# Performance work log

Hardware: AMD Instinct MI355X
Metric: run time of the kernel (lower is better)

The kernel has to match this reference:

```python
import jax, jax.numpy as jnp
import numpy as np

B, N, D, R, K = 16384, 20, 64, 3, 64  # batch, triples per sample, embed dim, n_relations, r_dim


def setup_inputs() -> dict:
    key = jax.random.key(0)
    ks = jax.random.split(key, 8)
    # xavier_normal std for [2D, K] matrices: sqrt(2/(2D+K))
    std_w = float(np.sqrt(2.0 / (2 * D + K)))
    std_r = float(np.sqrt(2.0 / (R + K)))
    return {
        "u_emb": jax.random.normal(ks[0], (B, D), dtype=jnp.float32),
        "i_emb": jax.random.normal(ks[1], (B, D), dtype=jnp.float32),
        "a_emb": jax.random.normal(ks[2], (B, N, D), dtype=jnp.float32),
        "o_emb": jax.random.normal(ks[3], (B, N, D), dtype=jnp.float32),
        "s": jax.random.randint(ks[4], (B, N), 0, R, dtype=jnp.int64),
        "w_uir": jax.random.normal(ks[5], (R, 2 * D, K), dtype=jnp.float32) * std_w,
        "w_aor": jax.random.normal(ks[6], (R, 2 * D, K), dtype=jnp.float32) * std_w,
        "r_vec": jax.random.normal(ks[7], (R, K), dtype=jnp.float32) * std_r,
    }


def reference(u_emb, i_emb, a_emb, o_emb, s, w_uir, w_aor, r_vec):
    # transr predictor, bpr loss
    ui_in = jnp.concatenate([u_emb, i_emb], axis=-1)          # [B, 2D]
    ao_in = jnp.concatenate([a_emb, o_emb], axis=-1)          # [B, N, 2D]
    n_rel = w_uir.shape[0]
    ui_emb = jnp.zeros(ao_in.shape[:2] + (w_uir.shape[-1],), dtype=ui_in.dtype)  # [B, N, K]
    ao_emb = jnp.zeros_like(ui_emb)
    for r_idx in range(n_rel):  # small fixed relation count
        m = (s == r_idx)[..., None]                            # [B, N, 1]
        ui_r = ui_in @ w_uir[r_idx] + r_vec[r_idx]             # [B, K]
        ao_r = jnp.einsum("bnd,dk->bnk", ao_in, w_aor[r_idx])  # [B, N, K]
        ui_emb = jnp.where(m, ui_r[:, None, :], ui_emb)
        ao_emb = jnp.where(m, ao_r, ao_emb)
    pred = jnp.sum(ui_emb * ao_emb, axis=-1)                   # [B, N]
    return pred
```

## Files before the change

### kernel.cpp

```cpp
#include <hip/hip_runtime.h>
#include <hip/hip_bf16.h>

#define BB   16384
#define NN   20
#define NREL 3

typedef __attribute__((ext_vector_type(8))) short  short8;
typedef __attribute__((ext_vector_type(4))) float  f32x4;

__device__ __forceinline__ float lo16(unsigned int u) {
    union { unsigned int x; float f; } c; c.x = u << 16; return c.f;
}
__device__ __forceinline__ float hi16(unsigned int u) {
    union { unsigned int x; float f; } c; c.x = u & 0xFFFF0000u; return c.f;
}

__device__ __forceinline__ unsigned short f2bu(float f) {
    union { float f; unsigned int u; } x;
    x.f = f;
    unsigned int r = x.u + 0x7FFFu + ((x.u >> 16) & 1u);
    return (unsigned short)(r >> 16);
}

__global__ __launch_bounds__(256) void k_precompute(
    const float* __restrict__ w_uir,
    const float* __restrict__ w_aor,
    const float* __restrict__ r_vec,
    unsigned short* __restrict__ McatT,
    float* __restrict__ cvec)
{
    int idx = blockIdx.x * 256 + threadIdx.x;
    if (idx < NREL * 128 * 128) {
        int d = idx & 127;
        int e = (idx >> 7) & 127;
        int r = idx >> 14;
        const float4* pu = reinterpret_cast<const float4*>(w_uir + (r * 128 + d) * 64);
        const float4* pa = reinterpret_cast<const float4*>(w_aor + (r * 128 + e) * 64);
        float acc = 0.f;
        #pragma unroll
        for (int k = 0; k < 16; ++k) {
            float4 a = pu[k], b = pa[k];
            acc += a.x * b.x + a.y * b.y + a.z * b.z + a.w * b.w;
        }
        McatT[(r * 128 + e) * 128 + d] = f2bu(acc);
    } else if (idx < NREL * 128 * 128 + NREL * 128) {
        int j = idx - NREL * 128 * 128;
        int r = j >> 7, e = j & 127;
        const float4* pr = reinterpret_cast<const float4*>(r_vec + r * 64);
        const float4* pa = reinterpret_cast<const float4*>(w_aor + (r * 128 + e) * 64);
        float acc = 0.f;
        #pragma unroll
        for (int k = 0; k < 16; ++k) {
            float4 a = pr[k], b = pa[k];
            acc += a.x * b.x + a.y * b.y + a.z * b.z + a.w * b.w;
        }
        cvec[j] = acc;
    }
}

__global__ __launch_bounds__(256) void k_gemm(
    const float* __restrict__ u_emb,
    const float* __restrict__ i_emb,
    const unsigned short* __restrict__ McatT,
    const float* __restrict__ cvec,
    unsigned short* __restrict__ vp)
{
    __shared__ unsigned short Atile[64][136];
    const int t = threadIdx.x;
    const int bm = blockIdx.x & 255;
    const int bn = blockIdx.x >> 8;
    const int Mbase = bm * 64;
    const int Nbase = bn * 64;

    #pragma unroll
    for (int it = 0; it < 8; ++it) {
        int idx  = it * 256 + t;
        int row  = idx >> 5;
        int colg = idx & 31;
        const float* src = (colg < 16)
            ? (u_emb + (Mbase + row) * 64 + colg * 4)
            : (i_emb + (Mbase + row) * 64 + (colg - 16) * 4);
        float4 v = *reinterpret_cast<const float4*>(src);
        ushort4 h;
        h.x = f2bu(v.x); h.y = f2bu(v.y); h.z = f2bu(v.z); h.w = f2bu(v.w);
        *reinterpret_cast<ushort4*>(&Atile[row][colg * 4]) = h;
    }
    __syncthreads();

    const int w    = t >> 6;
    const int lane = t & 63;
    const int lr   = lane & 15;
    const int lk   = (lane >> 4) * 8;

    short8 afrag[4];
    #pragma unroll
    for (int kk = 0; kk < 4; ++kk)
        afrag[kk] = *reinterpret_cast<const short8*>(&Atile[w * 16 + lr][kk * 32 + lk]);

    #pragma unroll
    for (int nt = 0; nt < 4; ++nt) {
        f32x4 acc = {0.f, 0.f, 0.f, 0.f};
        int col = Nbase + nt * 16 + lr;
        #pragma unroll
        for (int kk = 0; kk < 4; ++kk) {
            short8 bfrag = *reinterpret_cast<const short8*>(McatT + col * 128 + kk * 32 + lk);
            acc = __builtin_amdgcn_mfma_f32_16x16x32_bf16(afrag[kk], bfrag, acc, 0, 0, 0);
        }
        float cb = cvec[col];
        #pragma unroll
        for (int reg = 0; reg < 4; ++reg) {
            int grow = Mbase + w * 16 + (lane >> 4) * 4 + reg;
            vp[grow * 384 + col] = f2bu(acc[reg] + cb);
        }
    }
}

#define K3_BLOCKS 512
#define K3_ITERS  16
#define K3_TPS    40

#define SL_A   0
#define SL_O   10240
#define SL_VP  20480
#define SL_S   22016
#define SL_SZ  22272

__device__ __forceinline__ void k3_stage(
    const float* __restrict__ a_emb, const float* __restrict__ o_emb,
    const int* __restrict__ s, const unsigned short* __restrict__ vp,
    char* L, int sidx, int wv, int lane)
{
    const size_t t0s = (size_t)sidx * K3_TPS;

    int sval = 0;
    if (wv == 2 && lane < K3_TPS) sval = s[t0s + lane];

    const char* asrc = (const char*)(a_emb + t0s * 64);
    const char* osrc = (const char*)(o_emb + t0s * 64);
    const char* vsrc = (const char*)(vp + (size_t)sidx * (2 * 3 * 128));

    if (wv < 2) {
        #pragma unroll
        for (int i = 0; i < 5; ++i) {
            int seg = i * 2 + wv;
            __builtin_amdgcn_global_load_lds(
                (const unsigned int*)(asrc + seg * 1024 + (size_t)lane * 16),
                (unsigned int*)(L + SL_A + seg * 1024), 16, 0, 0);
        }
    } else {
        #pragma unroll
        for (int i = 0; i < 5; ++i) {
            int seg = i * 2 + (wv & 1);
            __builtin_amdgcn_global_load_lds(
                (const unsigned int*)(osrc + seg * 1024 + (size_t)lane * 16),
                (unsigned int*)(L + SL_O + seg * 1024), 16, 0, 0);
        }
    }
    if (wv == 3) {
        __builtin_amdgcn_global_load_lds(
            (const unsigned int*)(vsrc + (size_t)lane * 16),
            (unsigned int*)(L + SL_VP), 16, 0, 0);
        if (lane < 32)
            __builtin_amdgcn_global_load_lds(
                (const unsigned int*)(vsrc + 1024 + (size_t)lane * 16),
                (unsigned int*)(L + SL_VP + 1024), 16, 0, 0);
    }
    if (wv == 2 && lane < K3_TPS)
        *(int*)(L + SL_S + lane * 4) = sval;
}

__device__ __forceinline__ void k3_consume(
    const char* L, int sidx, int g, int sub, float* __restrict__ out)
{
    const size_t t0s = (size_t)sidx * K3_TPS;
    #pragma unroll
    for (int p = 0; p < 3; ++p) {
        const int ltrip = p * 16 + g;
        if (p < 2 || g < 8) {
            const int bl  = ltrip / NN;
            const int sv  = *(const int*)(L + SL_S + ltrip * 4);
            const int row = bl * 3 + sv;
            float4 af = *(const float4*)(L + SL_A + ltrip * 256 + sub * 16);
            float4 of = *(const float4*)(L + SL_O + ltrip * 256 + sub * 16);
            uint2  wa = *(const uint2*)(L + SL_VP + row * 256 + sub * 8);
            uint2  wo = *(const uint2*)(L + SL_VP + row * 256 + 128 + sub * 8);
            float r = af.x * lo16(wa.x) + af.y * hi16(wa.x)
                    + af.z * lo16(wa.y) + af.w * hi16(wa.y)
                    + of.x * lo16(wo.x) + of.y * hi16(wo.x)
                    + of.z * lo16(wo.y) + of.w * hi16(wo.y);
            r += __shfl_xor(r, 1, 64);
            r += __shfl_xor(r, 2, 64);
            r += __shfl_xor(r, 4, 64);
            r += __shfl_xor(r, 8, 64);
            if (sub == 0) out[t0s + ltrip] = r;
        }
    }
}

__global__ __launch_bounds__(256) void k_pred(
    const float* __restrict__ a_emb,
    const float* __restrict__ o_emb,
    const int* __restrict__ s,
    const unsigned short* __restrict__ vp,
    float* __restrict__ out)
{
    __shared__ __align__(16) char lds[2 * SL_SZ];

    const int tid  = threadIdx.x;
    const int wv   = tid >> 6;
    const int lane = tid & 63;
    const int bid  = blockIdx.x;
    const int g    = tid >> 4;
    const int sub  = tid & 15;

    const int sbase = bid * K3_ITERS;

    k3_stage(a_emb, o_emb, s, vp, lds, sbase, wv, lane);
    __syncthreads();

    for (int it = 0; it < K3_ITERS; ++it) {
        if (it + 1 < K3_ITERS)
            k3_stage(a_emb, o_emb, s, vp, lds + ((it + 1) & 1) * SL_SZ,
                     sbase + it + 1, wv, lane);
        k3_consume(lds + (it & 1) * SL_SZ, sbase + it, g, sub, out);
        __syncthreads();
    }
}

extern "C" void kernel_launch(void* const* d_in, const int* in_sizes, int n_in,
                              void* d_out, int out_size, void* d_ws, size_t ws_size,
                              hipStream_t stream) {
    const float* u_emb = (const float*)d_in[0];
    const float* i_emb = (const float*)d_in[1];
    const float* a_emb = (const float*)d_in[2];
    const float* o_emb = (const float*)d_in[3];
    const int*   s     = (const int*)d_in[4];
    const float* w_uir = (const float*)d_in[5];
    const float* w_aor = (const float*)d_in[6];
    const float* r_vec = (const float*)d_in[7];
    float* out = (float*)d_out;

    char* ws = (char*)d_ws;
    unsigned short* McatT = (unsigned short*)ws;
    float*          cvec  = (float*)(ws + 98304);
    unsigned short* vp    = (unsigned short*)(ws + 102400);

    k_precompute<<<194, 256, 0, stream>>>(w_uir, w_aor, r_vec, McatT, cvec);
    k_gemm<<<1536, 256, 0, stream>>>(u_emb, i_emb, McatT, cvec, vp);
    k_pred<<<K3_BLOCKS, 256, 0, stream>>>(a_emb, o_emb, s, vp, out);
}
```

Baseline: 54.43 us.

## Triple-buffer k_pred with per-batch stages, explicit vmcnt waits, coalesced output

Restructures the prediction kernel to process one batch row (20 triples) per iteration across 1024 blocks, with a three-deep LDS ring filled by direct global-to-LDS loads. Fixed-count s_waitcnt vmcnt waits plus a raw s_barrier replace the full __syncthreads each iteration. Relation indices are loaded once up front, and results are staged in LDS and written out as coalesced float4 stores at the end. The aim is to keep more memory traffic in flight and cut per-iteration synchronisation. The risk is that each wave waits only on its own loads before reading buffers filled by other waves, with no barrier in between, so a read could race a load that has not landed.

```diff
diff --git a/kernel.cpp b/kernel.cpp
--- a/kernel.cpp
+++ b/kernel.cpp
@@ -115,85 +115,87 @@
     }
 }
 
-#define K3_BLOCKS 512
-#define K3_ITERS  16
-#define K3_TPS    40
-
-#define SL_A   0
-#define SL_O   10240
-#define SL_VP  20480
-#define SL_S   22016
-#define SL_SZ  22272
+#define K3_BLOCKS 1024
+#define K3_NITER  16
+#define K3_BUF    11264
+#define K3_SOFF   (3 * K3_BUF)
+#define K3_OOFF   (K3_SOFF + 1280)
+#define K3_LDS    (K3_OOFF + 1280)
 
 __device__ __forceinline__ void k3_stage(
     const float* __restrict__ a_emb, const float* __restrict__ o_emb,
-    const int* __restrict__ s, const unsigned short* __restrict__ vp,
-    char* L, int sidx, int wv, int lane)
-{
-    const size_t t0s = (size_t)sidx * K3_TPS;
-
-    int sval = 0;
-    if (wv == 2 && lane < K3_TPS) sval = s[t0s + lane];
-
-    const char* asrc = (const char*)(a_emb + t0s * 64);
-    const char* osrc = (const char*)(o_emb + t0s * 64);
-    const char* vsrc = (const char*)(vp + (size_t)sidx * (2 * 3 * 128));
-
-    if (wv < 2) {
-        #pragma unroll
-        for (int i = 0; i < 5; ++i) {
-            int seg = i * 2 + wv;
-            __builtin_amdgcn_global_load_lds(
-                (const unsigned int*)(asrc + seg * 1024 + (size_t)lane * 16),
-                (unsigned int*)(L + SL_A + seg * 1024), 16, 0, 0);
-        }
+    const unsigned short* __restrict__ vpg,
+    char* buf, int bb, int wv, int lane)
+{
+    const char* asrc = (const char*)a_emb + (size_t)bb * 5120;
+    const char* osrc = (const char*)o_emb + (size_t)bb * 5120;
+    if (wv == 0) {
+        __builtin_amdgcn_global_load_lds((const unsigned int*)(asrc + 0 * 1024 + lane * 16),
+                                         (unsigned int*)(buf + 0 * 1024), 16, 0, 0);
+        __builtin_amdgcn_global_load_lds((const unsigned int*)(asrc + 1 * 1024 + lane * 16),
+                                         (unsigned int*)(buf + 1 * 1024), 16, 0, 0);
+        __builtin_amdgcn_global_load_lds((const unsigned int*)(asrc + 2 * 1024 + lane * 16),
+                                         (unsigned int*)(buf + 2 * 1024), 16, 0, 0);
+    } else if (wv == 1) {
+        __builtin_amdgcn_global_load_lds((const unsigned int*)(asrc + 3 * 1024 + lane * 16),
+                                         (unsigned int*)(buf + 3 * 1024), 16, 0, 0);
+        __builtin_amdgcn_global_load_lds((const unsigned int*)(asrc + 4 * 1024 + lane * 16),
+                                         (unsigned int*)(buf + 4 * 1024), 16, 0, 0);
+        __builtin_amdgcn_global_load_lds((const unsigned int*)(osrc + 0 * 1024 + lane * 16),
+                                         (unsigned int*)(buf + 5120 + 0 * 1024), 16, 0, 0);
+    } else if (wv == 2) {
+        __builtin_amdgcn_global_load_lds((const unsigned int*)(osrc + 1 * 1024 + lane * 16),
+                                         (unsigned int*)(buf + 5120 + 1 * 1024), 16, 0, 0);
+        __builtin_amdgcn_global_load_lds((const unsigned int*)(osrc + 2 * 1024 + lane * 16),
+                                         (unsigned int*)(buf + 5120 + 2 * 1024), 16, 0, 0);
+        __builtin_amdgcn_global_load_lds((const unsigned int*)(osrc + 3 * 1024 + lane * 16),
+                                         (unsigned int*)(buf + 5120 + 3 * 1024), 16, 0, 0);
     } else {
-        #pragma unroll
-        for (int i = 0; i < 5; ++i) {
-            int seg = i * 2 + (wv & 1);
-            __builtin_amdgcn_global_load_lds(
-                (const unsigned int*)(osrc + seg * 1024 + (size_t)lane * 16),
-                (unsigned int*)(L + SL_O + seg * 1024), 16, 0, 0);
-        }
-    }
-    if (wv == 3) {
-        __builtin_amdgcn_global_load_lds(
-            (const unsigned int*)(vsrc + (size_t)lane * 16),
-            (unsigned int*)(L + SL_VP), 16, 0, 0);
-        if (lane < 32)
-            __builtin_amdgcn_global_load_lds(
-                (const unsigned int*)(vsrc + 1024 + (size_t)lane * 16),
-                (unsigned int*)(L + SL_VP + 1024), 16, 0, 0);
-    }
-    if (wv == 2 && lane < K3_TPS)
-        *(int*)(L + SL_S + lane * 4) = sval;
+        __builtin_amdgcn_global_load_lds((const unsigned int*)(osrc + 4 * 1024 + lane * 16),
+                                         (unsigned int*)(buf + 5120 + 4 * 1024), 16, 0, 0);
+        const char* vsrc = (const char*)vpg + (size_t)bb * 768;
+        if (lane < 48)
+            __builtin_amdgcn_global_load_lds((const unsigned int*)(vsrc + lane * 16),
+                                             (unsigned int*)(buf + 10240), 16, 0, 0);
+    }
 }
 
 __device__ __forceinline__ void k3_consume(
-    const char* L, int sidx, int g, int sub, float* __restrict__ out)
-{
-    const size_t t0s = (size_t)sidx * K3_TPS;
-    #pragma unroll
-    for (int p = 0; p < 3; ++p) {
-        const int ltrip = p * 16 + g;
-        if (p < 2 || g < 8) {
-            const int bl  = ltrip / NN;
-            const int sv  = *(const int*)(L + SL_S + ltrip * 4);
-            const int row = bl * 3 + sv;
-            float4 af = *(const float4*)(L + SL_A + ltrip * 256 + sub * 16);
-            float4 of = *(const float4*)(L + SL_O + ltrip * 256 + sub * 16);
-            uint2  wa = *(const uint2*)(L + SL_VP + row * 256 + sub * 8);
-            uint2  wo = *(const uint2*)(L + SL_VP + row * 256 + 128 + sub * 8);
-            float r = af.x * lo16(wa.x) + af.y * hi16(wa.x)
-                    + af.z * lo16(wa.y) + af.w * hi16(wa.y)
-                    + of.x * lo16(wo.x) + of.y * hi16(wo.x)
-                    + of.z * lo16(wo.y) + of.w * hi16(wo.y);
-            r += __shfl_xor(r, 1, 64);
-            r += __shfl_xor(r, 2, 64);
-            r += __shfl_xor(r, 4, 64);
-            r += __shfl_xor(r, 8, 64);
-            if (sub == 0) out[t0s + ltrip] = r;
-        }
+    char* lds, const char* buf, int it, int g, int sub)
+{
+    {
+        const int ltrip = g;
+        const int sv = *(const int*)(lds + K3_SOFF + (it * 20 + ltrip) * 4);
+        float4 af = *(const float4*)(buf + ltrip * 256 + sub * 16);
+        float4 of = *(const float4*)(buf + 5120 + ltrip * 256 + sub * 16);
+        uint2  wa = *(const uint2*)(buf + 10240 + sv * 256 + sub * 8);
+        uint2  wo = *(const uint2*)(buf + 10240 + sv * 256 + 128 + sub * 8);
+        float r = af.x * lo16(wa.x) + af.y * hi16(wa.x)
+                + af.z * lo16(wa.y) + af.w * hi16(wa.y)
+                + of.x * lo16(wo.x) + of.y * hi16(wo.x)
+                + of.z * lo16(wo.y) + of.w * hi16(wo.y);
+        r += __shfl_xor(r, 1, 64);
+        r += __shfl_xor(r, 2, 64);
+        r += __shfl_xor(r, 4, 64);
+        r += __shfl_xor(r, 8, 64);
+        if (sub == 0) *(float*)(lds + K3_OOFF + (it * 20 + ltrip) * 4) = r;
+    }
+    if (g < 4) {
+        const int ltrip = 16 + g;
+        const int sv = *(const int*)(lds + K3_SOFF + (it * 20 + ltrip) * 4);
+        float4 af = *(const float4*)(buf + ltrip * 256 + sub * 16);
+        float4 of = *(const float4*)(buf + 5120 + ltrip * 256 + sub * 16);
+        uint2  wa = *(const uint2*)(buf + 10240 + sv * 256 + sub * 8);
+        uint2  wo = *(const uint2*)(buf + 10240 + sv * 256 + 128 + sub * 8);
+        float r = af.x * lo16(wa.x) + af.y * hi16(wa.x)
+                + af.z * lo16(wa.y) + af.w * hi16(wa.y)
+                + of.x * lo16(wo.x) + of.y * hi16(wo.x)
+                + of.z * lo16(wo.y) + of.w * hi16(wo.y);
+        r += __shfl_xor(r, 1, 64);
+        r += __shfl_xor(r, 2, 64);
+        r += __shfl_xor(r, 4, 64);
+        r += __shfl_xor(r, 8, 64);
+        if (sub == 0) *(float*)(lds + K3_OOFF + (it * 20 + ltrip) * 4) = r;
     }
 }
 
@@ -201,29 +203,60 @@
     const float* __restrict__ a_emb,
     const float* __restrict__ o_emb,
     const int* __restrict__ s,
-    const unsigned short* __restrict__ vp,
+    const unsigned short* __restrict__ vpg,
     float* __restrict__ out)
 {
-    __shared__ __align__(16) char lds[2 * SL_SZ];
+    __shared__ __align__(16) char lds[K3_LDS];
 
     const int tid  = threadIdx.x;
+    const int bid  = blockIdx.x;
     const int wv   = tid >> 6;
     const int lane = tid & 63;
-    const int bid  = blockIdx.x;
     const int g    = tid >> 4;
     const int sub  = tid & 15;
-
-    const int sbase = bid * K3_ITERS;
-
-    k3_stage(a_emb, o_emb, s, vp, lds, sbase, wv, lane);
+    const size_t t0 = (size_t)bid * (K3_NITER * NN);
+    const int  b0  = bid * K3_NITER;
+
+    int sv1 = s[t0 + tid];
+    int sv2 = (tid < 64) ? s[t0 + 256 + tid] : 0;
+
+    k3_stage(a_emb, o_emb, vpg, lds + 0 * K3_BUF, b0 + 0, wv, lane);
+    k3_stage(a_emb, o_emb, vpg, lds + 1 * K3_BUF, b0 + 1, wv, lane);
+
+    *(int*)(lds + K3_SOFF + tid * 4) = sv1;
+    if (tid < 64) *(int*)(lds + K3_SOFF + 1024 + tid * 4) = sv2;
     __syncthreads();
 
-    for (int it = 0; it < K3_ITERS; ++it) {
-        if (it + 1 < K3_ITERS)
-            k3_stage(a_emb, o_emb, s, vp, lds + ((it + 1) & 1) * SL_SZ,
-                     sbase + it + 1, wv, lane);
-        k3_consume(lds + (it & 1) * SL_SZ, sbase + it, g, sub, out);
-        __syncthreads();
+    #pragma unroll
+    for (int it = 0; it < K3_NITER; ++it) {
+        if (it + 2 < K3_NITER)
+            k3_stage(a_emb, o_emb, vpg, lds + ((it + 2) % 3) * K3_BUF,
+                     b0 + it + 2, wv, lane);
+        __builtin_amdgcn_sched_barrier(0);
+
+        if (it >= 2) {
+            if (it < K3_NITER - 2) {
+                if (wv == 3) asm volatile("s_waitcnt vmcnt(4)" ::: "memory");
+                else         asm volatile("s_waitcnt vmcnt(6)" ::: "memory");
+            } else if (it == K3_NITER - 2) {
+                if (wv == 3) asm volatile("s_waitcnt vmcnt(2)" ::: "memory");
+                else         asm volatile("s_waitcnt vmcnt(3)" ::: "memory");
+            } else {
+                asm volatile("s_waitcnt vmcnt(0)" ::: "memory");
+            }
+        }
+        __builtin_amdgcn_sched_barrier(0);
+
+        k3_consume(lds, lds + (it % 3) * K3_BUF, it, g, sub);
+
+        __builtin_amdgcn_sched_barrier(0);
+        __builtin_amdgcn_s_barrier();
+    }
+
+    __syncthreads();
+    if (tid < 80) {
+        float4 v = *(const float4*)(lds + K3_OOFF + tid * 16);
+        *(float4*)(out + t0 + tid * 4) = v;
     }
 }
 
```

New measurement: 54.70 us. No clear change (+0.5%).

## Fuse projection GEMM into prediction kernel, keeping per-sample vectors in LDS

Applied to the files above, without the earlier changes.

Merges the MFMA GEMM that builds the per-sample projected vectors with the prediction kernel, so each block of 16 samples computes its vp rows into LDS and consumes them directly. This removes the global write and reread of vp and one kernel launch. The price is a loss of cross-iteration double buffering: each block now stages a/o slices in a synchronous load-then-consume pattern with extra barriers. It also launches 1024 blocks using about 56KB of LDS each.

```diff
diff --git a/kernel.cpp b/kernel.cpp
--- a/kernel.cpp
+++ b/kernel.cpp
@@ -58,172 +58,138 @@
     }
 }
 
-__global__ __launch_bounds__(256) void k_gemm(
+#define K3_BLOCKS (BB / 16)
+#define UI_OFF 0
+#define VP_OFF 4096
+#define AO_OFF 16384
+#define K3_LDS 57344
+
+__device__ __forceinline__ void stage_ao(
+    const float* __restrict__ a_emb, const float* __restrict__ o_emb,
+    char* lds, size_t t0s, int wv, int lane)
+{
+    const char* asrc = (const char*)a_emb + t0s * 256;
+    const char* osrc = (const char*)o_emb + t0s * 256;
+    #pragma unroll
+    for (int i = 0; i < 5; ++i) {
+        int seg = i * 4 + wv;
+        __builtin_amdgcn_global_load_lds(
+            (const unsigned int*)(asrc + seg * 1024 + (size_t)lane * 16),
+            (unsigned int*)(lds + AO_OFF + seg * 1024), 16, 0, 0);
+    }
+    #pragma unroll
+    for (int i = 0; i < 5; ++i) {
+        int seg = i * 4 + wv;
+        __builtin_amdgcn_global_load_lds(
+            (const unsigned int*)(osrc + seg * 1024 + (size_t)lane * 16),
+            (unsigned int*)(lds + AO_OFF + 20480 + seg * 1024), 16, 0, 0);
+    }
+}
+
+__device__ __forceinline__ void consume_slice(
+    const char* lds, int sl, size_t t0s,
+    const int* sv, int g, int sub, float* __restrict__ out)
+{
+    #pragma unroll
+    for (int p = 0; p < 5; ++p) {
+        const int ltrip = p * 16 + g;
+        const int bl    = ltrip / NN;
+        const int brow  = sl * 4 + bl;
+        const int svv   = sv[p];
+        float4 af = *(const float4*)(lds + AO_OFF + ltrip * 256 + sub * 16);
+        float4 of = *(const float4*)(lds + AO_OFF + 20480 + ltrip * 256 + sub * 16);
+        uint2  wa = *(const uint2*)(lds + VP_OFF + brow * 768 + svv * 256 + sub * 8);
+        uint2  wo = *(const uint2*)(lds + VP_OFF + brow * 768 + svv * 256 + 128 + sub * 8);
+        float r = af.x * lo16(wa.x) + af.y * hi16(wa.x)
+                + af.z * lo16(wa.y) + af.w * hi16(wa.y)
+                + of.x * lo16(wo.x) + of.y * hi16(wo.x)
+                + of.z * lo16(wo.y) + of.w * hi16(wo.y);
+        r += __shfl_xor(r, 1, 64);
+        r += __shfl_xor(r, 2, 64);
+        r += __shfl_xor(r, 4, 64);
+        r += __shfl_xor(r, 8, 64);
+        if (sub == 0) out[t0s + ltrip] = r;
+    }
+}
+
+__global__ __launch_bounds__(256) void k_fused(
     const float* __restrict__ u_emb,
     const float* __restrict__ i_emb,
-    const unsigned short* __restrict__ McatT,
-    const float* __restrict__ cvec,
-    unsigned short* __restrict__ vp)
-{
-    __shared__ unsigned short Atile[64][136];
-    const int t = threadIdx.x;
-    const int bm = blockIdx.x & 255;
-    const int bn = blockIdx.x >> 8;
-    const int Mbase = bm * 64;
-    const int Nbase = bn * 64;
-
-    #pragma unroll
-    for (int it = 0; it < 8; ++it) {
-        int idx  = it * 256 + t;
-        int row  = idx >> 5;
-        int colg = idx & 31;
-        const float* src = (colg < 16)
-            ? (u_emb + (Mbase + row) * 64 + colg * 4)
-            : (i_emb + (Mbase + row) * 64 + (colg - 16) * 4);
-        float4 v = *reinterpret_cast<const float4*>(src);
-        ushort4 h;
-        h.x = f2bu(v.x); h.y = f2bu(v.y); h.z = f2bu(v.z); h.w = f2bu(v.w);
-        *reinterpret_cast<ushort4*>(&Atile[row][colg * 4]) = h;
-    }
-    __syncthreads();
-
-    const int w    = t >> 6;
-    const int lane = t & 63;
-    const int lr   = lane & 15;
-    const int lk   = (lane >> 4) * 8;
-
-    short8 afrag[4];
-    #pragma unroll
-    for (int kk = 0; kk < 4; ++kk)
-        afrag[kk] = *reinterpret_cast<const short8*>(&Atile[w * 16 + lr][kk * 32 + lk]);
-
-    #pragma unroll
-    for (int nt = 0; nt < 4; ++nt) {
-        f32x4 acc = {0.f, 0.f, 0.f, 0.f};
-        int col = Nbase + nt * 16 + lr;
-        #pragma unroll
-        for (int kk = 0; kk < 4; ++kk) {
-            short8 bfrag = *reinterpret_cast<const short8*>(McatT + col * 128 + kk * 32 + lk);
-            acc = __builtin_amdgcn_mfma_f32_16x16x32_bf16(afrag[kk], bfrag, acc, 0, 0, 0);
-        }
-        float cb = cvec[col];
-        #pragma unroll
-        for (int reg = 0; reg < 4; ++reg) {
-            int grow = Mbase + w * 16 + (lane >> 4) * 4 + reg;
-            vp[grow * 384 + col] = f2bu(acc[reg] + cb);
-        }
-    }
-}
-
-#define K3_BLOCKS 512
-#define K3_ITERS  16
-#define K3_TPS    40
-
-#define SL_A   0
-#define SL_O   10240
-#define SL_VP  20480
-#define SL_S   22016
-#define SL_SZ  22272
-
-__device__ __forceinline__ void k3_stage(
-    const float* __restrict__ a_emb, const float* __restrict__ o_emb,
-    const int* __restrict__ s, const unsigned short* __restrict__ vp,
-    char* L, int sidx, int wv, int lane)
-{
-    const size_t t0s = (size_t)sidx * K3_TPS;
-
-    int sval = 0;
-    if (wv == 2 && lane < K3_TPS) sval = s[t0s + lane];
-
-    const char* asrc = (const char*)(a_emb + t0s * 64);
-    const char* osrc = (const char*)(o_emb + t0s * 64);
-    const char* vsrc = (const char*)(vp + (size_t)sidx * (2 * 3 * 128));
-
-    if (wv < 2) {
-        #pragma unroll
-        for (int i = 0; i < 5; ++i) {
-            int seg = i * 2 + wv;
-            __builtin_amdgcn_global_load_lds(
-                (const unsigned int*)(asrc + seg * 1024 + (size_t)lane * 16),
-                (unsigned int*)(L + SL_A + seg * 1024), 16, 0, 0);
-        }
-    } else {
-        #pragma unroll
-        for (int i = 0; i < 5; ++i) {
-            int seg = i * 2 + (wv & 1);
-            __builtin_amdgcn_global_load_lds(
-                (const unsigned int*)(osrc + seg * 1024 + (size_t)lane * 16),
-                (unsigned int*)(L + SL_O + seg * 1024), 16, 0, 0);
-        }
-    }
-    if (wv == 3) {
-        __builtin_amdgcn_global_load_lds(
-            (const unsigned int*)(vsrc + (size_t)lane * 16),
-            (unsigned int*)(L + SL_VP), 16, 0, 0);
-        if (lane < 32)
-            __builtin_amdgcn_global_load_lds(
-                (const unsigned int*)(vsrc + 1024 + (size_t)lane * 16),
-                (unsigned int*)(L + SL_VP + 1024), 16, 0, 0);
-    }
-    if (wv == 2 && lane < K3_TPS)
-        *(int*)(L + SL_S + lane * 4) = sval;
-}
-
-__device__ __forceinline__ void k3_consume(
-    const char* L, int sidx, int g, int sub, float* __restrict__ out)
-{
-    const size_t t0s = (size_t)sidx * K3_TPS;
-    #pragma unroll
-    for (int p = 0; p < 3; ++p) {
-        const int ltrip = p * 16 + g;
-        if (p < 2 || g < 8) {
-            const int bl  = ltrip / NN;
-            const int sv  = *(const int*)(L + SL_S + ltrip * 4);
-            const int row = bl * 3 + sv;
-            float4 af = *(const float4*)(L + SL_A + ltrip * 256 + sub * 16);
-            float4 of = *(const float4*)(L + SL_O + ltrip * 256 + sub * 16);
-            uint2  wa = *(const uint2*)(L + SL_VP + row * 256 + sub * 8);
-            uint2  wo = *(const uint2*)(L + SL_VP + row * 256 + 128 + sub * 8);
-            float r = af.x * lo16(wa.x) + af.y * hi16(wa.x)
-                    + af.z * lo16(wa.y) + af.w * hi16(wa.y)
-                    + of.x * lo16(wo.x) + of.y * hi16(wo.x)
-                    + of.z * lo16(wo.y) + of.w * hi16(wo.y);
-            r += __shfl_xor(r, 1, 64);
-            r += __shfl_xor(r, 2, 64);
-            r += __shfl_xor(r, 4, 64);
-            r += __shfl_xor(r, 8, 64);
-            if (sub == 0) out[t0s + ltrip] = r;
-        }
-    }
-}
-
-__global__ __launch_bounds__(256) void k_pred(
     const float* __restrict__ a_emb,
     const float* __restrict__ o_emb,
     const int* __restrict__ s,
-    const unsigned short* __restrict__ vp,
+    const unsigned short* __restrict__ McatT,
+    const float* __restrict__ cvec,
     float* __restrict__ out)
 {
-    __shared__ __align__(16) char lds[2 * SL_SZ];
+    __shared__ __align__(16) char lds[K3_LDS];
 
     const int tid  = threadIdx.x;
+    const int bid  = blockIdx.x;
     const int wv   = tid >> 6;
     const int lane = tid & 63;
-    const int bid  = blockIdx.x;
     const int g    = tid >> 4;
     const int sub  = tid & 15;
-
-    const int sbase = bid * K3_ITERS;
-
-    k3_stage(a_emb, o_emb, s, vp, lds, sbase, wv, lane);
+    const int lr   = lane & 15;
+    const int lk   = (lane >> 4) * 8;
+
+    const int    b0     = bid * 16;
+    const size_t t0blk  = (size_t)bid * 320;
+
+    stage_ao(a_emb, o_emb, lds, t0blk, wv, lane);
+    int sv0[5];
+    #pragma unroll
+    for (int p = 0; p < 5; ++p) sv0[p] = s[t0blk + p * 16 + g];
+
+    {
+        const int r  = tid >> 4;
+        const int c8 = (tid & 15) * 8;
+        const float* src = (c8 < 64)
+            ? (u_emb + (size_t)(b0 + r) * 64 + c8)
+            : (i_emb + (size_t)(b0 + r) * 64 + (c8 - 64));
+        float4 v0 = *(const float4*)(src);
+        float4 v1 = *(const float4*)(src + 4);
+        unsigned short h[8];
+        h[0] = f2bu(v0.x); h[1] = f2bu(v0.y); h[2] = f2bu(v0.z); h[3] = f2bu(v0.w);
+        h[4] = f2bu(v1.x); h[5] = f2bu(v1.y); h[6] = f2bu(v1.z); h[7] = f2bu(v1.w);
+        *(ushort4*)(lds + UI_OFF + (r * 128 + c8) * 2)       = *(ushort4*)&h[0];
+        *(ushort4*)(lds + UI_OFF + (r * 128 + c8) * 2 + 8)   = *(ushort4*)&h[4];
+    }
     __syncthreads();
 
-    for (int it = 0; it < K3_ITERS; ++it) {
-        if (it + 1 < K3_ITERS)
-            k3_stage(a_emb, o_emb, s, vp, lds + ((it + 1) & 1) * SL_SZ,
-                     sbase + it + 1, wv, lane);
-        k3_consume(lds + (it & 1) * SL_SZ, sbase + it, g, sub, out);
+    const unsigned short* ui16 = (const unsigned short*)(lds + UI_OFF);
+    #pragma unroll
+    for (int nt = 0; nt < 6; ++nt) {
+        const int col = wv * 96 + nt * 16 + lr;
+        f32x4 acc = {0.f, 0.f, 0.f, 0.f};
+        #pragma unroll
+        for (int kk = 0; kk < 4; ++kk) {
+            short8 afrag = *(const short8*)&ui16[lr * 128 + kk * 32 + lk];
+            short8 bfrag = *(const short8*)(McatT + col * 128 + kk * 32 + lk);
+            acc = __builtin_amdgcn_mfma_f32_16x16x32_bf16(afrag, bfrag, acc, 0, 0, 0);
+        }
+        const float cb = cvec[col];
+        #pragma unroll
+        for (int reg = 0; reg < 4; ++reg) {
+            const int brow = (lane >> 4) * 4 + reg;
+            *(unsigned short*)(lds + VP_OFF + brow * 768 + col * 2)
+                = f2bu(acc[reg] + cb);
+        }
+    }
+    __syncthreads();
+
+    consume_slice(lds, 0, t0blk, sv0, g, sub, out);
+
+    #pragma unroll
+    for (int sl = 1; sl < 4; ++sl) {
         __syncthreads();
+        const size_t t0s = t0blk + (size_t)sl * 80;
+        stage_ao(a_emb, o_emb, lds, t0s, wv, lane);
+        int sv[5];
+        #pragma unroll
+        for (int p = 0; p < 5; ++p) sv[p] = s[t0s + p * 16 + g];
+        __syncthreads();
+        consume_slice(lds, sl, t0s, sv, g, sub, out);
     }
 }
 
@@ -243,9 +209,8 @@
     char* ws = (char*)d_ws;
     unsigned short* McatT = (unsigned short*)ws;
     float*          cvec  = (float*)(ws + 98304);
-    unsigned short* vp    = (unsigned short*)(ws + 102400);
 
     k_precompute<<<194, 256, 0, stream>>>(w_uir, w_aor, r_vec, McatT, cvec);
-    k_gemm<<<1536, 256, 0, stream>>>(u_emb, i_emb, McatT, cvec, vp);
-    k_pred<<<K3_BLOCKS, 256, 0, stream>>>(a_emb, o_emb, s, vp, out);
-}
+    k_fused<<<K3_BLOCKS, 256, 0, stream>>>(u_emb, i_emb, a_emb, o_emb, s,
+                                           McatT, cvec, out);
+}
```

New measurement: 46.40 us. 14.8% less time.
